# Optimization experiments

Hardware: AMD Instinct MI355X
Metric: run time of the kernel (lower is better)

The kernel has to match this reference:

```python
import jax, jax.numpy as jnp
import numpy as np

NUM_GRAPHS = 128

def setup_inputs() -> dict:
    key = jax.random.key(0)
    k1, k2, k3, k4, k5, k6 = jax.random.split(key, 6)
    N, E, H = 100000, 3200000, 256
    x = jax.random.normal(k1, (N, 1), dtype=jnp.float32)
    edge_index = jax.random.randint(k2, (2, E), 0, N, dtype=jnp.int64)
    batch = jnp.sort(jax.random.randint(k3, (N,), 0, NUM_GRAPHS, dtype=jnp.int64))
    # SAGEConv lin_l: [in=1 -> out=H], plus bias; final Linear [H -> 1]
    W_l = jax.random.normal(k4, (1, H), dtype=jnp.float32) / jnp.sqrt(1.0)
    b_l = jnp.zeros((H,), dtype=jnp.float32)
    W_out = jax.random.normal(k5, (H, 1), dtype=jnp.float32) / jnp.sqrt(H)
    b_out = jax.random.normal(k6, (1,), dtype=jnp.float32) * 0.01
    return {"x": x, "edge_index": edge_index, "batch": batch,
            "W_l": W_l, "b_l": b_l, "W_out": W_out, "b_out": b_out}

def reference(x, edge_index, batch, W_l, b_l, W_out, b_out):
    N = x.shape[0]
    src, dst = edge_index[0], edge_index[1]
    # SAGEConv(aggr='sum', root_weight=False): agg[i] = sum_{j->i} x[j]; out = agg @ W_l + b_l
    agg = jax.ops.segment_sum(x[src], dst, num_segments=N)  # [N,1]
    h = agg @ W_l + b_l                                      # [N,H]
    h = jax.nn.relu(h)
    # global_mean_pool over batch ids
    sums = jax.ops.segment_sum(h, batch, num_segments=NUM_GRAPHS)          # [G,H]
    counts = jax.ops.segment_sum(jnp.ones((N,), h.dtype), batch, num_segments=NUM_GRAPHS)
    pooled = sums / jnp.maximum(counts, 1.0)[:, None]
    out = pooled @ W_out + b_out                             # [G,1]
    return jax.nn.relu(out)
```

## Files before the change

### kernel.cpp

```cpp
#include <hip/hip_runtime.h>


#define GMAX  128
#define HMAX  256
#define BS    256
#define NBMAX 512
#define SG    512
#define BLK2  512
#define CEDGE 6400


__global__ __launch_bounds__(256) void s1_count(const int* __restrict__ ei,
                                                unsigned* __restrict__ cnt,
                                                int E, int NB, int QpB) {
  __shared__ unsigned h[NBMAX];
  int tid = threadIdx.x;
  for (int b = tid; b < NB; b += 256) h[b] = 0u;
  __syncthreads();
  int Q = E >> 2;
  int q0 = blockIdx.x * QpB;
  int q1 = min(q0 + QpB, Q);
  const int4* d4 = (const int4*)(ei + E);
  for (int q = q0 + tid; q < q1; q += 256) {
    int4 d = d4[q];
    atomicAdd(&h[d.x >> 8], 1u);
    atomicAdd(&h[d.y >> 8], 1u);
    atomicAdd(&h[d.z >> 8], 1u);
    atomicAdd(&h[d.w >> 8], 1u);
  }
  if (blockIdx.x == 0)
    for (int e = (Q << 2) + tid; e < E; e += 256)
      atomicAdd(&h[ei[E + e] >> 8], 1u);
  __syncthreads();
  for (int b = tid; b < NB; b += 256)
    cnt[(size_t)blockIdx.x * NBMAX + b] = h[b];
}

__global__ __launch_bounds__(SG) void s_scan(const unsigned* __restrict__ cnt,
                                             unsigned* __restrict__ off,
                                             unsigned* __restrict__ tot,
                                             float* __restrict__ gsum,
                                             float* __restrict__ gcnt,
                                             unsigned* __restrict__ done) {
  __shared__ unsigned s[SG];
  int b = blockIdx.x, t = threadIdx.x;
  unsigned c = cnt[(size_t)t * NBMAX + b];
  s[t] = c;
  __syncthreads();
  for (int o = 1; o < SG; o <<= 1) {
    unsigned v = (t >= o) ? s[t - o] : 0u;
    __syncthreads();
    s[t] += v;
    __syncthreads();
  }
  off[(size_t)t * NBMAX + b] = s[t] - c;
  if (t == SG - 1) tot[b] = s[t];
  if (b == 0) {
    if (t < GMAX) { gsum[t] = 0.f; gcnt[t] = 0.f; }
    if (t == 0) done[0] = 0u;
  }
}

__global__ __launch_bounds__(BLK2) void s2_scatter(const int* __restrict__ ei,
                                                   const unsigned* __restrict__ cnt,
                                                   const unsigned* __restrict__ off,
                                                   unsigned* __restrict__ pairs,
                                                   int E, int NB, int QpB, int CAP) {
  __shared__ unsigned lp[CEDGE];
  __shared__ unsigned short lb[CEDGE];
  __shared__ unsigned lbase[NBMAX];
  __shared__ unsigned lrank[NBMAX];
  __shared__ unsigned hb[NBMAX];
  __shared__ unsigned sc[NBMAX];
  int tid = threadIdx.x, blk = blockIdx.x;

  for (int b = tid; b < NBMAX; b += BLK2) {
    unsigned c = (b < NB) ? cnt[(size_t)blk * NBMAX + b] : 0u;
    sc[b] = c;
    lrank[b] = 0u;
    if (b < NB) hb[b] = (unsigned)b * (unsigned)CAP + off[(size_t)blk * NBMAX + b];
  }
  __syncthreads();
  for (int o = 1; o < NBMAX; o <<= 1) {
    unsigned v = 0u;
    if (tid < NBMAX && tid >= o) v = sc[tid - o];
    __syncthreads();
    if (tid < NBMAX) sc[tid] += v;
    __syncthreads();
  }
  for (int b = tid; b < NB; b += BLK2) {
    unsigned c = cnt[(size_t)blk * NBMAX + b];
    lbase[b] = sc[b] - c;
  }
  __syncthreads();

  int Q = E >> 2;
  int q0 = blk * QpB;
  int q1 = min(q0 + QpB, Q);
  const int4* s4 = (const int4*)ei;
  const int4* d4 = (const int4*)(ei + E);
  for (int q = q0 + tid; q < q1; q += BLK2) {
    int4 s = s4[q];
    int4 d = d4[q];
    { int b = d.x >> 8; unsigned r = atomicAdd(&lrank[b], 1u);
      unsigned p = lbase[b] + r;
      lp[p] = ((unsigned)s.x << 8) | (unsigned)(d.x & 255); lb[p] = (unsigned short)b; }
    { int b = d.y >> 8; unsigned r = atomicAdd(&lrank[b], 1u);
      unsigned p = lbase[b] + r;
      lp[p] = ((unsigned)s.y << 8) | (unsigned)(d.y & 255); lb[p] = (unsigned short)b; }
    { int b = d.z >> 8; unsigned r = atomicAdd(&lrank[b], 1u);
      unsigned p = lbase[b] + r;
      lp[p] = ((unsigned)s.z << 8) | (unsigned)(d.z & 255); lb[p] = (unsigned short)b; }
    { int b = d.w >> 8; unsigned r = atomicAdd(&lrank[b], 1u);
      unsigned p = lbase[b] + r;
      lp[p] = ((unsigned)s.w << 8) | (unsigned)(d.w & 255); lb[p] = (unsigned short)b; }
  }
  int total = (q1 - q0) * 4;
  if (blk == 0) {
    for (int e = (Q << 2) + tid; e < E; e += BLK2) {
      int d = ei[E + e], s = ei[e];
      int b = d >> 8; unsigned r = atomicAdd(&lrank[b], 1u);
      unsigned p = lbase[b] + r;
      lp[p] = ((unsigned)s << 8) | (unsigned)(d & 255); lb[p] = (unsigned short)b;
    }
    total += (E & 3);
  }
  if (total > CEDGE) total = CEDGE;
  __syncthreads();

  unsigned capu = (unsigned)CAP;
  for (int i = tid; i < total; i += BLK2) {
    unsigned b = lb[i];
    unsigned slot = hb[b] + ((unsigned)i - lbase[b]);
    if (slot < (b + 1u) * capu)
      pairs[slot] = lp[i];
  }
}

__global__ __launch_bounds__(1024) void s3_reduce(
    const unsigned* __restrict__ pairs, const unsigned* __restrict__ tot,
    const float* __restrict__ x, const int* __restrict__ batch,
    const float* __restrict__ Wl, const float* __restrict__ bl,
    const float* __restrict__ Wo, const float* __restrict__ b_out,
    float* __restrict__ gsum, float* __restrict__ gcnt,
    unsigned* __restrict__ done, float* __restrict__ out,
    int N, int H, int G, int CAP) {
  __shared__ float acc[BS];
  __shared__ float sWl[HMAX], sbl[HMAX], sWo[HMAX];
  __shared__ float ls[GMAX], lc[GMAX];
  __shared__ unsigned ticket;
  int tid = threadIdx.x, b = blockIdx.x;
  if (tid < BS) acc[tid] = 0.f;
  if (tid < H) { sWl[tid] = Wl[tid]; sbl[tid] = bl[tid]; sWo[tid] = Wo[tid]; }
  if (tid < GMAX) { ls[tid] = 0.f; lc[tid] = 0.f; }
  __syncthreads();

  unsigned lo = (unsigned)b * (unsigned)CAP;
  unsigned cnt = min(tot[b], (unsigned)CAP);
  unsigned q4 = cnt >> 2;
  const uint4* p4 = (const uint4*)(pairs + lo);
  for (unsigned i = tid; i < q4; i += 1024) {
    uint4 p = p4[i];
    atomicAdd(&acc[p.x & 255u], x[p.x >> 8]);
    atomicAdd(&acc[p.y & 255u], x[p.y >> 8]);
    atomicAdd(&acc[p.z & 255u], x[p.z >> 8]);
    atomicAdd(&acc[p.w & 255u], x[p.w >> 8]);
  }
  if (tid < (int)(cnt & 3u)) {
    unsigned p = pairs[lo + (q4 << 2) + tid];
    atomicAdd(&acc[p & 255u], x[p >> 8]);
  }
  __syncthreads();

  int node = b * BS + tid;
  if (tid < BS && node < N) {
    float a = acc[tid], f = 0.f;
#pragma unroll 8
    for (int k = 0; k < H; ++k) {
      float hh = fmaf(a, sWl[k], sbl[k]);
      f = fmaf(fmaxf(hh, 0.f), sWo[k], f);
    }
    int g = batch[node];
    atomicAdd(&ls[g], f);
    atomicAdd(&lc[g], 1.f);
  }
  __syncthreads();
  if (tid < GMAX && lc[tid] != 0.f) {
    atomicAdd(&gsum[tid], ls[tid]);
    atomicAdd(&gcnt[tid], lc[tid]);
  }
  __syncthreads();
  if (tid == 0)
    ticket = __hip_atomic_fetch_add(done, 1u, __ATOMIC_ACQ_REL,
                                    __HIP_MEMORY_SCOPE_AGENT);
  __syncthreads();
  if (ticket == gridDim.x - 1 && tid < G) {
    float s = __hip_atomic_load(&gsum[tid], __ATOMIC_RELAXED, __HIP_MEMORY_SCOPE_AGENT);
    float c = __hip_atomic_load(&gcnt[tid], __ATOMIC_RELAXED, __HIP_MEMORY_SCOPE_AGENT);
    out[tid] = fmaxf(s / fmaxf(c, 1.f) + b_out[0], 0.f);
  }
}


__global__ __launch_bounds__(256) void fb_scatter(const int* __restrict__ ei,
                                                  const float* __restrict__ x,
                                                  float* __restrict__ agg, int E) {
  int t = blockIdx.x * blockDim.x + threadIdx.x;
  if (t < E) atomicAdd(&agg[ei[E + t]], x[ei[t]]);
}

__global__ __launch_bounds__(256) void fb_node(const float* __restrict__ agg,
                                               const int* __restrict__ batch,
                                               const float* __restrict__ Wl,
                                               const float* __restrict__ bl,
                                               const float* __restrict__ Wo,
                                               float* __restrict__ gsum,
                                               float* __restrict__ gcnt, int N, int H) {
  __shared__ float sWl[HMAX], sbl[HMAX], sWo[HMAX];
  __shared__ float ls[GMAX], lc[GMAX];
  int tid = threadIdx.x;
  if (tid < H) { sWl[tid] = Wl[tid]; sbl[tid] = bl[tid]; sWo[tid] = Wo[tid]; }
  if (tid < GMAX) { ls[tid] = 0.f; lc[tid] = 0.f; }
  __syncthreads();
  int i = blockIdx.x * blockDim.x + tid;
  if (i < N) {
    float a = agg[i], f = 0.f;
    for (int k = 0; k < H; ++k) {
      float hh = fmaf(a, sWl[k], sbl[k]);
      f = fmaf(fmaxf(hh, 0.f), sWo[k], f);
    }
    int g = batch[i];
    atomicAdd(&ls[g], f);
    atomicAdd(&lc[g], 1.f);
  }
  __syncthreads();
  if (tid < GMAX && lc[tid] != 0.f) {
    atomicAdd(&gsum[tid], ls[tid]);
    atomicAdd(&gcnt[tid], lc[tid]);
  }
}

__global__ void fb_final(const float* __restrict__ gsum,
                         const float* __restrict__ gcnt,
                         const float* __restrict__ b_out,
                         float* __restrict__ out, int G) {
  int g = blockIdx.x * blockDim.x + threadIdx.x;
  if (g < G) out[g] = fmaxf(gsum[g] / fmaxf(gcnt[g], 1.f) + b_out[0], 0.f);
}


extern "C" void kernel_launch(void* const* d_in, const int* in_sizes, int n_in,
                              void* d_out, int out_size, void* d_ws, size_t ws_size,
                              hipStream_t stream) {
  const float* x     = (const float*)d_in[0];
  const int*   ei    = (const int*)d_in[1];
  const int*   batch = (const int*)d_in[2];
  const float* Wl    = (const float*)d_in[3];
  const float* bl    = (const float*)d_in[4];
  const float* Wo    = (const float*)d_in[5];
  const float* bo    = (const float*)d_in[6];
  float* out = (float*)d_out;

  int N = in_sizes[0];
  int E = in_sizes[1] / 2;
  int H = in_sizes[3];
  int G = out_size;

  int NB = (N + BS - 1) / BS;
  int Q   = E >> 2;
  int QpB = (Q + SG - 1) / SG;

  int avg = (NB > 0) ? E / NB : 0;
  int CAP = (2 * avg + 4095) & ~4095;
  if (CAP < 4096) CAP = 4096;

  const size_t W_MAT = (size_t)SG * NBMAX;
  const size_t HDRW  = 2 * W_MAT + NBMAX + 2 * GMAX + 4;
  size_t need = (HDRW + (size_t)NB * (size_t)CAP) * 4u;

  unsigned* w = (unsigned*)d_ws;
  if (NB <= NBMAX && ws_size >= need && H <= HMAX && G <= GMAX &&
      QpB * 4 + 4 <= CEDGE) {
    unsigned* cnt   = w;
    unsigned* off   = cnt + W_MAT;
    unsigned* tot   = off + W_MAT;
    float*    gsum  = (float*)(tot + NBMAX);
    float*    gcnt  = gsum + GMAX;
    unsigned* done  = (unsigned*)(gcnt + GMAX);
    unsigned* pairs = done + 4;

    s1_count<<<SG, 256, 0, stream>>>(ei, cnt, E, NB, QpB);
    s_scan<<<NB, SG, 0, stream>>>(cnt, off, tot, gsum, gcnt, done);
    s2_scatter<<<SG, BLK2, 0, stream>>>(ei, cnt, off, pairs, E, NB, QpB, CAP);
    s3_reduce<<<NB, 1024, 0, stream>>>(pairs, tot, x, batch, Wl, bl, Wo, bo,
                                       gsum, gcnt, done, out, N, H, G, CAP);
  } else {
    float* agg  = (float*)d_ws;
    float* gsum = agg + N;
    float* gcnt = gsum + GMAX;
    hipMemsetAsync(d_ws, 0, ((size_t)N + 2 * GMAX) * 4u, stream);
    fb_scatter<<<(E + 255) / 256, 256, 0, stream>>>(ei, x, agg, E);
    fb_node<<<(N + 255) / 256, 256, 0, stream>>>(agg, batch, Wl, bl, Wo,
                                                 gsum, gcnt, N, H);
    fb_final<<<1, 256, 0, stream>>>(gsum, gcnt, bo, out, G);
  }
}
```

Measured before the change: 131.9 us.

## Fuse count, scan and scatter into one kernel using global atomic bucket offsets

Replaces the separate per-block histogram kernel and the cross-block prefix-scan kernel with a single sort kernel. Each block builds its local bucket histogram, then reserves a contiguous range in each bucket with one global atomicAdd on a padded counter, and scatters its edges. This removes two kernel launches and the large count/offset matrices in global memory, at the cost of a memset, contended global atomics per bucket, and a nondeterministic edge order within each bucket.

```diff
diff --git a/kernel.cpp b/kernel.cpp
--- a/kernel.cpp
+++ b/kernel.cpp
@@ -8,78 +8,44 @@
 #define SG    512
 #define BLK2  512
 #define CEDGE 6400
-
-
-__global__ __launch_bounds__(256) void s1_count(const int* __restrict__ ei,
-                                                unsigned* __restrict__ cnt,
-                                                int E, int NB, int QpB) {
-  __shared__ unsigned h[NBMAX];
-  int tid = threadIdx.x;
-  for (int b = tid; b < NB; b += 256) h[b] = 0u;
-  __syncthreads();
-  int Q = E >> 2;
-  int q0 = blockIdx.x * QpB;
-  int q1 = min(q0 + QpB, Q);
-  const int4* d4 = (const int4*)(ei + E);
-  for (int q = q0 + tid; q < q1; q += 256) {
-    int4 d = d4[q];
-    atomicAdd(&h[d.x >> 8], 1u);
-    atomicAdd(&h[d.y >> 8], 1u);
-    atomicAdd(&h[d.z >> 8], 1u);
-    atomicAdd(&h[d.w >> 8], 1u);
-  }
-  if (blockIdx.x == 0)
-    for (int e = (Q << 2) + tid; e < E; e += 256)
-      atomicAdd(&h[ei[E + e] >> 8], 1u);
-  __syncthreads();
-  for (int b = tid; b < NB; b += 256)
-    cnt[(size_t)blockIdx.x * NBMAX + b] = h[b];
-}
-
-__global__ __launch_bounds__(SG) void s_scan(const unsigned* __restrict__ cnt,
-                                             unsigned* __restrict__ off,
-                                             unsigned* __restrict__ tot,
-                                             float* __restrict__ gsum,
-                                             float* __restrict__ gcnt,
-                                             unsigned* __restrict__ done) {
-  __shared__ unsigned s[SG];
-  int b = blockIdx.x, t = threadIdx.x;
-  unsigned c = cnt[(size_t)t * NBMAX + b];
-  s[t] = c;
-  __syncthreads();
-  for (int o = 1; o < SG; o <<= 1) {
-    unsigned v = (t >= o) ? s[t - o] : 0u;
-    __syncthreads();
-    s[t] += v;
-    __syncthreads();
-  }
-  off[(size_t)t * NBMAX + b] = s[t] - c;
-  if (t == SG - 1) tot[b] = s[t];
-  if (b == 0) {
-    if (t < GMAX) { gsum[t] = 0.f; gcnt[t] = 0.f; }
-    if (t == 0) done[0] = 0u;
-  }
-}
-
-__global__ __launch_bounds__(BLK2) void s2_scatter(const int* __restrict__ ei,
-                                                   const unsigned* __restrict__ cnt,
-                                                   const unsigned* __restrict__ off,
-                                                   unsigned* __restrict__ pairs,
-                                                   int E, int NB, int QpB, int CAP) {
+#define RSTR  16
+
+
+__global__ __launch_bounds__(BLK2) void s2_sort(const int* __restrict__ ei,
+                                                unsigned* __restrict__ grank,
+                                                unsigned* __restrict__ pairs,
+                                                int E, int NB, int QpB, int CAP) {
   __shared__ unsigned lp[CEDGE];
   __shared__ unsigned short lb[CEDGE];
+  __shared__ unsigned hist[NBMAX];
+  __shared__ unsigned sc[NBMAX];
   __shared__ unsigned lbase[NBMAX];
   __shared__ unsigned lrank[NBMAX];
   __shared__ unsigned hb[NBMAX];
-  __shared__ unsigned sc[NBMAX];
   int tid = threadIdx.x, blk = blockIdx.x;
 
-  for (int b = tid; b < NBMAX; b += BLK2) {
-    unsigned c = (b < NB) ? cnt[(size_t)blk * NBMAX + b] : 0u;
-    sc[b] = c;
-    lrank[b] = 0u;
-    if (b < NB) hb[b] = (unsigned)b * (unsigned)CAP + off[(size_t)blk * NBMAX + b];
-  }
+  for (int b = tid; b < NBMAX; b += BLK2) { hist[b] = 0u; lrank[b] = 0u; }
+  __syncthreads();
+
+  int Q = E >> 2;
+  int q0 = blk * QpB;
+  int q1 = min(q0 + QpB, Q);
+  const int4* s4 = (const int4*)ei;
+  const int4* d4 = (const int4*)(ei + E);
+
+  for (int q = q0 + tid; q < q1; q += BLK2) {
+    int4 d = d4[q];
+    atomicAdd(&hist[d.x >> 8], 1u);
+    atomicAdd(&hist[d.y >> 8], 1u);
+    atomicAdd(&hist[d.z >> 8], 1u);
+    atomicAdd(&hist[d.w >> 8], 1u);
+  }
+  if (blk == 0)
+    for (int e = (Q << 2) + tid; e < E; e += BLK2)
+      atomicAdd(&hist[ei[E + e] >> 8], 1u);
+  __syncthreads();
+
+  for (int b = tid; b < NBMAX; b += BLK2) sc[b] = hist[b];
   __syncthreads();
   for (int o = 1; o < NBMAX; o <<= 1) {
     unsigned v = 0u;
@@ -89,16 +55,13 @@
     __syncthreads();
   }
   for (int b = tid; b < NB; b += BLK2) {
-    unsigned c = cnt[(size_t)blk * NBMAX + b];
+    unsigned c = hist[b];
     lbase[b] = sc[b] - c;
-  }
-  __syncthreads();
-
-  int Q = E >> 2;
-  int q0 = blk * QpB;
-  int q1 = min(q0 + QpB, Q);
-  const int4* s4 = (const int4*)ei;
-  const int4* d4 = (const int4*)(ei + E);
+    unsigned r = c ? atomicAdd(&grank[(size_t)b * RSTR], c) : 0u;
+    hb[b] = (unsigned)b * (unsigned)CAP + r;
+  }
+  __syncthreads();
+
   for (int q = q0 + tid; q < q1; q += BLK2) {
     int4 s = s4[q];
     int4 d = d4[q];
@@ -138,7 +101,7 @@
 }
 
 __global__ __launch_bounds__(1024) void s3_reduce(
-    const unsigned* __restrict__ pairs, const unsigned* __restrict__ tot,
+    const unsigned* __restrict__ pairs, const unsigned* __restrict__ grank,
     const float* __restrict__ x, const int* __restrict__ batch,
     const float* __restrict__ Wl, const float* __restrict__ bl,
     const float* __restrict__ Wo, const float* __restrict__ b_out,
@@ -156,7 +119,7 @@
   __syncthreads();
 
   unsigned lo = (unsigned)b * (unsigned)CAP;
-  unsigned cnt = min(tot[b], (unsigned)CAP);
+  unsigned cnt = min(grank[(size_t)b * RSTR], (unsigned)CAP);
   unsigned q4 = cnt >> 2;
   const uint4* p4 = (const uint4*)(pairs + lo);
   for (unsigned i = tid; i < q4; i += 1024) {
@@ -274,25 +237,21 @@
   int CAP = (2 * avg + 4095) & ~4095;
   if (CAP < 4096) CAP = 4096;
 
-  const size_t W_MAT = (size_t)SG * NBMAX;
-  const size_t HDRW  = 2 * W_MAT + NBMAX + 2 * GMAX + 4;
+  const size_t HDRW = (size_t)NBMAX * RSTR + 2 * GMAX + 4;
   size_t need = (HDRW + (size_t)NB * (size_t)CAP) * 4u;
 
   unsigned* w = (unsigned*)d_ws;
   if (NB <= NBMAX && ws_size >= need && H <= HMAX && G <= GMAX &&
       QpB * 4 + 4 <= CEDGE) {
-    unsigned* cnt   = w;
-    unsigned* off   = cnt + W_MAT;
-    unsigned* tot   = off + W_MAT;
-    float*    gsum  = (float*)(tot + NBMAX);
+    unsigned* grank = w;
+    float*    gsum  = (float*)(grank + (size_t)NBMAX * RSTR);
     float*    gcnt  = gsum + GMAX;
     unsigned* done  = (unsigned*)(gcnt + GMAX);
     unsigned* pairs = done + 4;
 
-    s1_count<<<SG, 256, 0, stream>>>(ei, cnt, E, NB, QpB);
-    s_scan<<<NB, SG, 0, stream>>>(cnt, off, tot, gsum, gcnt, done);
-    s2_scatter<<<SG, BLK2, 0, stream>>>(ei, cnt, off, pairs, E, NB, QpB, CAP);
-    s3_reduce<<<NB, 1024, 0, stream>>>(pairs, tot, x, batch, Wl, bl, Wo, bo,
+    hipMemsetAsync(d_ws, 0, HDRW * 4u, stream);
+    s2_sort<<<SG, BLK2, 0, stream>>>(ei, grank, pairs, E, NB, QpB, CAP);
+    s3_reduce<<<NB, 1024, 0, stream>>>(pairs, grank, x, batch, Wl, bl, Wo, bo,
                                        gsum, gcnt, done, out, N, H, G, CAP);
   } else {
     float* agg  = (float*)d_ws;
```

Result: slower. 135.8 us (+3.0%).
